# Optimization experiments

Hardware: AMD Instinct MI355X
Metric: run time of the kernel (lower is better)

Reference implementation:

```python
import jax, jax.numpy as jnp
import numpy as np

B = 8388608
TRANSLATION_WEIGHT = 1.0
ROTATION_WEIGHT = 1.0


def setup_inputs() -> dict:
    key = jax.random.key(0)
    k1, k2 = jax.random.split(key)
    prediction = jax.random.normal(k1, (B, 7), dtype=jnp.float32)
    target = jax.random.normal(k2, (B, 7), dtype=jnp.float32)
    return {"prediction": prediction, "target": target}


def _geodesic_loss(q_pred, q_tgt):
    # scipy R.from_quat normalizes quaternions; relative rotation angle
    # magnitude(q_pred^-1 * q_tgt) = 2 * arccos(|<q_pred_hat, q_tgt_hat>|), in [0, pi]
    qp = q_pred / jnp.linalg.norm(q_pred, axis=-1, keepdims=True)
    qt = q_tgt / jnp.linalg.norm(q_tgt, axis=-1, keepdims=True)
    dot = jnp.abs(jnp.sum(qp * qt, axis=-1))
    angle = 2.0 * jnp.arccos(jnp.clip(dot, 0.0, 1.0))
    return jnp.mean(angle * angle)


def reference(prediction, target):
    t_pred, t_tgt = prediction[:, :3], target[:, :3]
    q_pred, q_tgt = prediction[:, 3:], target[:, 3:]
    translation_loss = jnp.mean((t_pred - t_tgt) ** 2)
    rotation_loss = _geodesic_loss(q_pred, q_tgt)
    return TRANSLATION_WEIGHT * translation_loss + ROTATION_WEIGHT * rotation_loss
```

## Files before the change

kernel.cpp:

```cpp
#include <hip/hip_runtime.h>


__global__ __launch_bounds__(256) void trl_partial_kernel(
    const float* __restrict__ pred,
    const float* __restrict__ targ,
    float* __restrict__ partial,
    int ngroups,
    float inv3B,
    float invB)
{
    const float4* __restrict__ p4 = (const float4*)pred;
    const float4* __restrict__ t4 = (const float4*)targ;

    int tid    = blockIdx.x * blockDim.x + threadIdx.x;
    int stride = gridDim.x * blockDim.x;

    float tsum = 0.0f;
    float rsum = 0.0f;

    for (int g = tid; g < ngroups; g += stride) {
        float4 pa[7], ta[7];
        const long base = 7L * g;
#pragma unroll
        for (int k = 0; k < 7; ++k) pa[k] = p4[base + k];
#pragma unroll
        for (int k = 0; k < 7; ++k) ta[k] = t4[base + k];

        const float* pv = (const float*)pa;
        const float* tv = (const float*)ta;

#pragma unroll
        for (int j = 0; j < 4; ++j) {
            const float* p = pv + 7 * j;
            const float* t = tv + 7 * j;

            float d0 = p[0] - t[0];
            float d1 = p[1] - t[1];
            float d2 = p[2] - t[2];
            tsum += d0 * d0 + d1 * d1 + d2 * d2;

            float np2 = p[3] * p[3] + p[4] * p[4] + p[5] * p[5] + p[6] * p[6];
            float nt2 = t[3] * t[3] + t[4] * t[4] + t[5] * t[5] + t[6] * t[6];
            float dot = p[3] * t[3] + p[4] * t[4] + p[5] * t[5] + p[6] * t[6];
            float c = fabsf(dot) * rsqrtf(np2 * nt2);
            c = fminf(c, 1.0f);
            float ang = 2.0f * acosf(c);
            rsum += ang * ang;
        }
    }

    float local = tsum * inv3B + rsum * invB;

#pragma unroll
    for (int off = 32; off > 0; off >>= 1)
        local += __shfl_down(local, off, 64);

    __shared__ float sdata[4];
    int lane = threadIdx.x & 63;
    int wave = threadIdx.x >> 6;
    if (lane == 0) sdata[wave] = local;
    __syncthreads();
    if (threadIdx.x == 0)
        partial[blockIdx.x] = sdata[0] + sdata[1] + sdata[2] + sdata[3];
}

__global__ __launch_bounds__(256) void trl_final_kernel(
    const float* __restrict__ partial, int n, float* __restrict__ out)
{
    float s = 0.0f;
    for (int i = threadIdx.x; i < n; i += 256) s += partial[i];
#pragma unroll
    for (int off = 32; off > 0; off >>= 1)
        s += __shfl_down(s, off, 64);
    __shared__ float sd[4];
    if ((threadIdx.x & 63) == 0) sd[threadIdx.x >> 6] = s;
    __syncthreads();
    if (threadIdx.x == 0) out[0] = sd[0] + sd[1] + sd[2] + sd[3];
}

extern "C" void kernel_launch(void* const* d_in, const int* in_sizes, int n_in,
                              void* d_out, int out_size, void* d_ws, size_t ws_size,
                              hipStream_t stream) {
    const float* pred = (const float*)d_in[0];
    const float* targ = (const float*)d_in[1];
    float* out = (float*)d_out;
    float* partial = (float*)d_ws;

    long long total = in_sizes[0];
    int B = (int)(total / 7);
    int ngroups = B / 4;

    float invB  = 1.0f / (float)B;
    float inv3B = invB / 3.0f;

    const int block = 256;
    const int grid  = 2048;

    trl_partial_kernel<<<grid, block, 0, stream>>>(pred, targ, partial, ngroups, inv3B, invB);
    trl_final_kernel<<<1, block, 0, stream>>>(partial, grid, out);
}
```

Baseline: 455.5 us.

## Stage input tiles through LDS for coalesced global loads

Each block now cooperatively loads a contiguous tile of prediction and target float4s into shared memory with coalesced accesses. Threads then read their 7 float4 groups from LDS, replacing strided per-thread global reads. A tail loop in block 0 handles leftover groups. The cost is 56KB of LDS per block, which lowers occupancy, plus two barriers per tile and possible LDS bank conflicts.

```diff
diff --git a/kernel.cpp b/kernel.cpp
--- a/kernel.cpp
+++ b/kernel.cpp
@@ -1,10 +1,14 @@
 #include <hip/hip_runtime.h>
 
 
-__global__ __launch_bounds__(256) void trl_partial_kernel(
+#define TILE_F4 1792
+#define BLOCK 256
+
+__global__ __launch_bounds__(BLOCK) void trl_partial_kernel(
     const float* __restrict__ pred,
     const float* __restrict__ targ,
     float* __restrict__ partial,
+    int ntiles,
     int ngroups,
     float inv3B,
     float invB)
@@ -12,23 +16,33 @@
     const float4* __restrict__ p4 = (const float4*)pred;
     const float4* __restrict__ t4 = (const float4*)targ;
 
-    int tid    = blockIdx.x * blockDim.x + threadIdx.x;
-    int stride = gridDim.x * blockDim.x;
+    __shared__ float4 sp[TILE_F4];
+    __shared__ float4 st[TILE_F4];
+
+    const int tid = threadIdx.x;
 
     float tsum = 0.0f;
     float rsum = 0.0f;
 
-    for (int g = tid; g < ngroups; g += stride) {
+    for (int tile = blockIdx.x; tile < ntiles; tile += gridDim.x) {
+        const int base = tile * TILE_F4;
+
+#pragma unroll
+        for (int j = 0; j < 7; ++j) {
+            const int idx = j * BLOCK + tid;
+            sp[idx] = p4[base + idx];
+            st[idx] = t4[base + idx];
+        }
+        __syncthreads();
+
         float4 pa[7], ta[7];
-        const long base = 7L * g;
 #pragma unroll
-        for (int k = 0; k < 7; ++k) pa[k] = p4[base + k];
+        for (int k = 0; k < 7; ++k) pa[k] = sp[7 * tid + k];
 #pragma unroll
-        for (int k = 0; k < 7; ++k) ta[k] = t4[base + k];
+        for (int k = 0; k < 7; ++k) ta[k] = st[7 * tid + k];
 
         const float* pv = (const float*)pa;
         const float* tv = (const float*)ta;
-
 #pragma unroll
         for (int j = 0; j < 4; ++j) {
             const float* p = pv + 7 * j;
@@ -46,6 +60,33 @@
             c = fminf(c, 1.0f);
             float ang = 2.0f * acosf(c);
             rsum += ang * ang;
+        }
+        __syncthreads();
+    }
+
+    if (blockIdx.x == 0) {
+        for (int g = ntiles * BLOCK + tid; g < ngroups; g += BLOCK) {
+            float4 pa[7], ta[7];
+            const long b = 7L * g;
+#pragma unroll
+            for (int k = 0; k < 7; ++k) pa[k] = p4[b + k];
+#pragma unroll
+            for (int k = 0; k < 7; ++k) ta[k] = t4[b + k];
+            const float* pv = (const float*)pa;
+            const float* tv = (const float*)ta;
+#pragma unroll
+            for (int j = 0; j < 4; ++j) {
+                const float* p = pv + 7 * j;
+                const float* t = tv + 7 * j;
+                float d0 = p[0] - t[0], d1 = p[1] - t[1], d2 = p[2] - t[2];
+                tsum += d0 * d0 + d1 * d1 + d2 * d2;
+                float np2 = p[3]*p[3] + p[4]*p[4] + p[5]*p[5] + p[6]*p[6];
+                float nt2 = t[3]*t[3] + t[4]*t[4] + t[5]*t[5] + t[6]*t[6];
+                float dot = p[3]*t[3] + p[4]*t[4] + p[5]*t[5] + p[6]*t[6];
+                float c = fminf(fabsf(dot) * rsqrtf(np2 * nt2), 1.0f);
+                float ang = 2.0f * acosf(c);
+                rsum += ang * ang;
+            }
         }
     }
 
@@ -89,13 +130,13 @@
     long long total = in_sizes[0];
     int B = (int)(total / 7);
     int ngroups = B / 4;
+    int ntiles = ngroups / BLOCK;
 
     float invB  = 1.0f / (float)B;
     float inv3B = invB / 3.0f;
 
-    const int block = 256;
-    const int grid  = 2048;
+    const int grid = 2048;
 
-    trl_partial_kernel<<<grid, block, 0, stream>>>(pred, targ, partial, ngroups, inv3B, invB);
-    trl_final_kernel<<<1, block, 0, stream>>>(partial, grid, out);
+    trl_partial_kernel<<<grid, BLOCK, 0, stream>>>(pred, targ, partial, ntiles, ngroups, inv3B, invB);
+    trl_final_kernel<<<1, BLOCK, 0, stream>>>(partial, grid, out);
 }
```

Result: no change. 449.3 us (-1.4%).
